# Kernel tuning notes

Measured on AMD Instinct MI355X. Metric: run time of the kernel, lower is better.

## Reference

```python
import jax, jax.numpy as jnp
import numpy as np

HEADS = 8
DIM_HEAD = 64
EPS = 1e-5

def setup_inputs() -> dict:
    key = jax.random.key(0)
    ks = jax.random.split(key, 5)
    c, inner = 320, HEADS * DIM_HEAD
    s = 0.02
    return {
        "hidden_states": jax.random.normal(ks[0], (4, c, 16, 32, 32), jnp.float32),
        "ln_w": jnp.ones((c,), jnp.float32),
        "ln_b": jnp.zeros((c,), jnp.float32),
        "Wq": jax.random.normal(ks[1], (inner, c), jnp.float32) * s,
        "Wk": jax.random.normal(ks[2], (inner, c), jnp.float32) * s,
        "Wv": jax.random.normal(ks[3], (inner, c), jnp.float32) * s,
        "Wo": jax.random.normal(ks[4], (c, inner), jnp.float32) * s,
        "bo": jnp.zeros((c,), jnp.float32),
    }

def reference(hidden_states, ln_w, ln_b, Wq, Wk, Wv, Wo, bo):
    b, c, t, h, w = hidden_states.shape
    scale = DIM_HEAD ** (-0.5)
    # (b h w) t c
    x0 = jnp.transpose(hidden_states, (0, 3, 4, 2, 1)).reshape(b * h * w, t, c)
    # LayerNorm over channel dim
    mu = jnp.mean(x0, axis=-1, keepdims=True)
    var = jnp.var(x0, axis=-1, keepdims=True)
    xn = (x0 - mu) / jnp.sqrt(var + EPS) * ln_w + ln_b
    # QKV projections (self-attention: encoder_hidden_states = normed hidden)
    q = xn @ Wq.T  # [B, t, inner]
    k = xn @ Wk.T
    v = xn @ Wv.T
    B = b * h * w
    q = q.reshape(B, t, HEADS, DIM_HEAD)
    k = k.reshape(B, t, HEADS, DIM_HEAD)
    v = v.reshape(B, t, HEADS, DIM_HEAD)
    scores = jnp.einsum("bqhd,bkhd->bhqk", q, k) * scale
    probs = jax.nn.softmax(scores, axis=-1)
    out = jnp.einsum("bhqk,bkhd->bqhd", probs, v).reshape(B, t, HEADS * DIM_HEAD)
    out = out @ Wo.T + bo
    out = out + x0  # residual (dropout p=0)
    # back to b c t h w
    return jnp.transpose(out.reshape(b, h, w, t, c), (0, 4, 3, 1, 2))
```

## Files before the change

kernel.cpp:

```cpp
#include <hip/hip_runtime.h>

#define TT 16
#define CC 320
#define NHEADS 8
#define DH 64
#define INNER 512

typedef float f32x4 __attribute__((ext_vector_type(4)));
typedef short bf16x8 __attribute__((ext_vector_type(8)));
typedef unsigned short u16;

__device__ __forceinline__ float bf2f(u16 u){
    union { unsigned int i; float f; } v; v.i = ((unsigned int)u) << 16; return v.f;
}
__device__ __forceinline__ u16 f2bf(float f){
    union { float f; unsigned int i; } v; v.f = f;
    unsigned int x = v.i;
    return (u16)((x + 0x7fffu + ((x >> 16) & 1u)) >> 16);
}

__global__ __launch_bounds__(256) void k_w2bf(const float* __restrict__ wq, const float* __restrict__ wk,
                                              const float* __restrict__ wv, const float* __restrict__ wo,
                                              u16* __restrict__ oq, u16* __restrict__ ok,
                                              u16* __restrict__ ov, u16* __restrict__ oo){
    const float* s; u16* d;
    switch (blockIdx.y){
        case 0: s = wq; d = oq; break;
        case 1: s = wk; d = ok; break;
        case 2: s = wv; d = ov; break;
        default: s = wo; d = oo; break;
    }
    int i = (blockIdx.x * 256 + threadIdx.x) * 4;
    f32x4 v = *(const f32x4*)(s + i);
    d[i + 0] = f2bf(v[0]); d[i + 1] = f2bf(v[1]);
    d[i + 2] = f2bf(v[2]); d[i + 3] = f2bf(v[3]);
}

__global__ __launch_bounds__(256) void k_ln(const float* __restrict__ x, const float* __restrict__ lnw,
                                            const float* __restrict__ lnb, u16* __restrict__ xn){
    __shared__ float tile[CC][37];
    __shared__ float psum[32][36];
    __shared__ float psq[32][36];
    __shared__ float meanb[32];
    __shared__ float rstdb[32];

    int wg = blockIdx.x;
    int t = wg & 15, h = (wg >> 4) & 31, b = wg >> 9;
    int tid = threadIdx.x;
    const size_t base = ((size_t)(b * CC) * TT + t) * 1024 + h * 32;

    int w4 = (tid & 7) * 4, cg = tid >> 3;
    f32x4 s4 = {0.f,0.f,0.f,0.f}, q4 = {0.f,0.f,0.f,0.f};
    for (int i = 0; i < 10; ++i){
        int c = cg * 10 + i;
        f32x4 v = *(const f32x4*)(x + base + (size_t)c * 16384 + w4);
        tile[c][w4 + 0] = v[0]; tile[c][w4 + 1] = v[1];
        tile[c][w4 + 2] = v[2]; tile[c][w4 + 3] = v[3];
        s4 += v; q4 += v * v;
    }
    psum[cg][w4 + 0] = s4[0]; psum[cg][w4 + 1] = s4[1]; psum[cg][w4 + 2] = s4[2]; psum[cg][w4 + 3] = s4[3];
    psq [cg][w4 + 0] = q4[0]; psq [cg][w4 + 1] = q4[1]; psq [cg][w4 + 2] = q4[2]; psq [cg][w4 + 3] = q4[3];
    __syncthreads();

    if (tid < 32){
        float s = 0.f, q = 0.f;
        for (int g = 0; g < 32; ++g){ s += psum[g][tid]; q += psq[g][tid]; }
        float mean = s * (1.f / CC);
        float var  = q * (1.f / CC) - mean * mean;
        meanb[tid] = mean;
        rstdb[tid] = rsqrtf(var + 1e-5f);
    }
    __syncthreads();

    int cl = tid & 63, wq_ = tid >> 6;
    float lw[5], lb[5];
    #pragma unroll
    for (int ci = 0; ci < 5; ++ci){ lw[ci] = lnw[ci * 64 + cl]; lb[ci] = lnb[ci * 64 + cl]; }
    int s_base = (b * 32 + h) * 32;
    for (int wi = 0; wi < 8; ++wi){
        int w = wq_ * 8 + wi;
        float mean = meanb[w], rstd = rstdb[w];
        size_t rowoff = ((size_t)(s_base + w) * TT + t) * CC;
        #pragma unroll
        for (int ci = 0; ci < 5; ++ci){
            int c = ci * 64 + cl;
            float nv = (tile[c][w] - mean) * rstd * lw[ci] + lb[ci];
            xn[rowoff + c] = f2bf(nv);
        }
    }
}

__global__ __launch_bounds__(256, 2) void k_attn(const u16* __restrict__ xng,
                                                 const u16* __restrict__ wq, const u16* __restrict__ wk,
                                                 const u16* __restrict__ wv, const u16* __restrict__ wo,
                                                 const float* __restrict__ bo, u16* __restrict__ proj){
    __shared__ u16 xn_s[64][328];
    __shared__ u16 qh_s[64][72];
    __shared__ u16 kh_s[64][72];
    __shared__ u16 vt_s[64][88];
    __shared__ u16 p_s[4][16][40];

    int tid = threadIdx.x;
    int lane = tid & 63;
    int wid = tid >> 6;
    int l15 = lane & 15;
    int g4  = lane >> 4;
    int s0 = blockIdx.x * 4;

    {
        const u16* src = xng + (size_t)s0 * TT * CC;
        #pragma unroll
        for (int i = 0; i < 10; ++i){
            int ch = tid + 256 * i;
            int r = ch / 40, cc8 = (ch % 40) * 8;
            *(bf16x8*)(&xn_s[r][cc8]) = *(const bf16x8*)(src + r * CC + cc8);
        }
        #pragma unroll
        for (int i = 0; i < 4; ++i){
            int idx = tid + 256 * i;
            vt_s[idx >> 4][64 + (idx & 15)] = 0;
        }
        #pragma unroll
        for (int i = 0; i < 4; ++i){
            int idx = tid + 256 * i;
            int wgg = idx >> 8, rest = idx & 255;
            p_s[wgg][rest >> 4][16 + (rest & 15)] = 0;
        }
    }
    __syncthreads();

    f32x4 acco[5][4];
    #pragma unroll
    for (int j = 0; j < 5; ++j)
        #pragma unroll
        for (int mb = 0; mb < 4; ++mb) acco[j][mb] = (f32x4){0.f,0.f,0.f,0.f};

    const f32x4 zero4 = (f32x4){0.f,0.f,0.f,0.f};

    for (int hd = 0; hd < NHEADS; ++hd){
        f32x4 aq[4], ak[4], av[4];
        #pragma unroll
        for (int mb = 0; mb < 4; ++mb){ aq[mb] = zero4; ak[mb] = zero4; av[mb] = zero4; }
        const u16* wqrow = wq + ((size_t)(hd * DH + wid * 16 + l15)) * CC + g4 * 8;
        const u16* wkrow = wk + ((size_t)(hd * DH + wid * 16 + l15)) * CC + g4 * 8;
        const u16* wvrow = wv + ((size_t)(hd * DH + wid * 16 + l15)) * CC + g4 * 8;
        for (int k0 = 0; k0 < CC; k0 += 32){
            bf16x8 bq = *(const bf16x8*)(wqrow + k0);
            bf16x8 bk = *(const bf16x8*)(wkrow + k0);
            bf16x8 aw = *(const bf16x8*)(wvrow + k0);
            #pragma unroll
            for (int mb = 0; mb < 4; ++mb){
                bf16x8 xa = *(const bf16x8*)(&xn_s[mb * 16 + l15][k0 + g4 * 8]);
                aq[mb] = __builtin_amdgcn_mfma_f32_16x16x32_bf16(xa, bq, aq[mb], 0, 0, 0);
                ak[mb] = __builtin_amdgcn_mfma_f32_16x16x32_bf16(xa, bk, ak[mb], 0, 0, 0);
                av[mb] = __builtin_amdgcn_mfma_f32_16x16x32_bf16(aw, xa, av[mb], 0, 0, 0);
            }
        }
        #pragma unroll
        for (int mb = 0; mb < 4; ++mb){
            #pragma unroll
            for (int r = 0; r < 4; ++r){
                int row = mb * 16 + g4 * 4 + r;
                qh_s[row][wid * 16 + l15] = f2bf(aq[mb][r] * 0.125f);
                kh_s[row][wid * 16 + l15] = f2bf(ak[mb][r]);
                vt_s[wid * 16 + g4 * 4 + r][mb * 16 + l15] = f2bf(av[mb][r]);
            }
        }
        __syncthreads();

        f32x4 sc = zero4;
        #pragma unroll
        for (int k0 = 0; k0 < DH; k0 += 32){
            bf16x8 qa = *(const bf16x8*)(&qh_s[wid * 16 + l15][k0 + g4 * 8]);
            bf16x8 kb = *(const bf16x8*)(&kh_s[wid * 16 + l15][k0 + g4 * 8]);
            sc = __builtin_amdgcn_mfma_f32_16x16x32_bf16(qa, kb, sc, 0, 0, 0);
        }
        f32x4 pr;
        #pragma unroll
        for (int r = 0; r < 4; ++r){
            float m = sc[r];
            m = fmaxf(m, __shfl_xor(m, 1)); m = fmaxf(m, __shfl_xor(m, 2));
            m = fmaxf(m, __shfl_xor(m, 4)); m = fmaxf(m, __shfl_xor(m, 8));
            float e = __expf(sc[r] - m);
            float s = e;
            s += __shfl_xor(s, 1); s += __shfl_xor(s, 2);
            s += __shfl_xor(s, 4); s += __shfl_xor(s, 8);
            pr[r] = e / s;
        }
        #pragma unroll
        for (int r = 0; r < 4; ++r) p_s[wid][g4 * 4 + r][l15] = f2bf(pr[r]);

        bf16x8 pa = *(const bf16x8*)(&p_s[wid][l15][g4 * 8]);
        f32x4 at[4];
        #pragma unroll
        for (int nb = 0; nb < 4; ++nb){
            bf16x8 vb = *(const bf16x8*)(&vt_s[nb * 16 + l15][wid * 16 + g4 * 8]);
            at[nb] = __builtin_amdgcn_mfma_f32_16x16x32_bf16(pa, vb, zero4, 0, 0, 0);
        }
        __syncthreads();
        #pragma unroll
        for (int nb = 0; nb < 4; ++nb)
            #pragma unroll
            for (int r = 0; r < 4; ++r)
                qh_s[wid * 16 + g4 * 4 + r][nb * 16 + l15] = f2bf(at[nb][r]);
        __syncthreads();

        #pragma unroll
        for (int k0 = 0; k0 < DH; k0 += 32){
            bf16x8 af[4];
            #pragma unroll
            for (int mb = 0; mb < 4; ++mb)
                af[mb] = *(const bf16x8*)(&qh_s[mb * 16 + l15][k0 + g4 * 8]);
            #pragma unroll
            for (int j = 0; j < 5; ++j){
                bf16x8 bw = *(const bf16x8*)(wo + ((size_t)((wid * 5 + j) * 16 + l15)) * INNER + hd * DH + k0 + g4 * 8);
                #pragma unroll
                for (int mb = 0; mb < 4; ++mb)
                    acco[j][mb] = __builtin_amdgcn_mfma_f32_16x16x32_bf16(af[mb], bw, acco[j][mb], 0, 0, 0);
            }
        }
        __syncthreads();
    }

    #pragma unroll
    for (int j = 0; j < 5; ++j){
        int c = (wid * 5 + j) * 16 + l15;
        float bias = bo[c];
        #pragma unroll
        for (int mb = 0; mb < 4; ++mb){
            size_t rowbase = ((size_t)(s0 + mb) * TT) * CC;
            #pragma unroll
            for (int r = 0; r < 4; ++r){
                int t = g4 * 4 + r;
                proj[rowbase + (size_t)t * CC + c] = f2bf(acco[j][mb][r] + bias);
            }
        }
    }
}

__global__ __launch_bounds__(256) void k_res(const u16* __restrict__ proj, const float* __restrict__ x,
                                             float* __restrict__ out){
    __shared__ u16 tile[32][328];
    int wg = blockIdx.x;
    int t = wg & 15, h = (wg >> 4) & 31, b = wg >> 9;
    int tid = threadIdx.x;
    int s0 = (b * 32 + h) * 32;
    #pragma unroll
    for (int i = 0; i < 5; ++i){
        int ch = tid + 256 * i;
        int w = ch / 40, cc8 = (ch % 40) * 8;
        *(bf16x8*)(&tile[w][cc8]) = *(const bf16x8*)(proj + ((size_t)(s0 + w) * TT + t) * CC + cc8);
    }
    __syncthreads();
    int w = tid & 31, cq = tid >> 5;
    size_t base = ((size_t)(b * CC) * TT + t) * 1024 + h * 32 + w;
    for (int i = 0; i < 40; ++i){
        int c = cq * 40 + i;
        size_t idx = base + (size_t)c * 16384;
        out[idx] = x[idx] + bf2f(tile[w][c]);
    }
}

extern "C" void kernel_launch(void* const* d_in, const int* in_sizes, int n_in,
                              void* d_out, int out_size, void* d_ws, size_t ws_size,
                              hipStream_t stream){
    const float* hid = (const float*)d_in[0];
    const float* lnw = (const float*)d_in[1];
    const float* lnb = (const float*)d_in[2];
    const float* Wq  = (const float*)d_in[3];
    const float* Wk  = (const float*)d_in[4];
    const float* Wv  = (const float*)d_in[5];
    const float* Wo  = (const float*)d_in[6];
    const float* bo  = (const float*)d_in[7];

    char* ws = (char*)d_ws;
    const size_t WN = 163840;
    u16* wq_b = (u16*)ws;
    u16* wk_b = wq_b + WN;
    u16* wv_b = wk_b + WN;
    u16* wo_b = wv_b + WN;
    u16* xn   = wo_b + WN;
    u16* proj = xn + (size_t)4096 * TT * CC;

    k_w2bf<<<dim3(160, 4), 256, 0, stream>>>(Wq, Wk, Wv, Wo, wq_b, wk_b, wv_b, wo_b);
    k_ln  <<<2048, 256, 0, stream>>>(hid, lnw, lnb, xn);
    k_attn<<<1024, 256, 0, stream>>>(xn, wq_b, wk_b, wv_b, wo_b, bo, proj);
    k_res <<<2048, 256, 0, stream>>>(proj, hid, (float*)d_out);
}
```

Measured before the change: 232.3 us.

## Retile attention kernel to 512 threads with register-resident xn fragments

The fused attention kernel now handles 8 sequences (128 rows) per 512-thread block. Each wave keeps its 32 rows of normalized input as register fragments, so there is no shared-memory staging of xn. Each wave computes a 32x32 tile of Q/K/V per head, which raises weight reuse per load. The per-head barrier count drops from four to three by writing the attention output into the K buffer, and the output projection is split into two column halves per wave. This costs many more registers per thread (20 A fragments plus 20 output accumulators) under a 2-blocks-per-CU bound of 512 threads, which risks spills or lower occupancy.

```diff
diff --git a/kernel.cpp b/kernel.cpp
--- a/kernel.cpp
+++ b/kernel.cpp
@@ -90,150 +90,177 @@
     }
 }
 
-__global__ __launch_bounds__(256, 2) void k_attn(const u16* __restrict__ xng,
+__global__ __launch_bounds__(512, 2) void k_attn(const u16* __restrict__ xng,
                                                  const u16* __restrict__ wq, const u16* __restrict__ wk,
                                                  const u16* __restrict__ wv, const u16* __restrict__ wo,
                                                  const float* __restrict__ bo, u16* __restrict__ proj){
-    __shared__ u16 xn_s[64][328];
-    __shared__ u16 qh_s[64][72];
-    __shared__ u16 kh_s[64][72];
-    __shared__ u16 vt_s[64][88];
-    __shared__ u16 p_s[4][16][40];
+    __shared__ u16 qh_s[128][76];
+    __shared__ u16 kh_s[128][76];
+    __shared__ u16 vt_s[64][148];
+    __shared__ u16 p_s[8][16][40];
 
     int tid = threadIdx.x;
     int lane = tid & 63;
     int wid = tid >> 6;
     int l15 = lane & 15;
     int g4  = lane >> 4;
-    int s0 = blockIdx.x * 4;
-
+    int mh = wid >> 1;
+    int nq = wid & 1;
+    const size_t mbase = (size_t)blockIdx.x * 128;
+
+    for (int i = tid; i < 64 * 20; i += 512) vt_s[i / 20][128 + i % 20] = 0;
+    for (int i = tid; i < 8 * 16 * 16; i += 512){
+        int w = i >> 8, rest = i & 255;
+        p_s[w][rest >> 4][16 + (rest & 15)] = 0;
+    }
+
+    bf16x8 a_f[2][10];
     {
-        const u16* src = xng + (size_t)s0 * TT * CC;
-        #pragma unroll
-        for (int i = 0; i < 10; ++i){
-            int ch = tid + 256 * i;
-            int r = ch / 40, cc8 = (ch % 40) * 8;
-            *(bf16x8*)(&xn_s[r][cc8]) = *(const bf16x8*)(src + r * CC + cc8);
-        }
-        #pragma unroll
-        for (int i = 0; i < 4; ++i){
-            int idx = tid + 256 * i;
-            vt_s[idx >> 4][64 + (idx & 15)] = 0;
-        }
-        #pragma unroll
-        for (int i = 0; i < 4; ++i){
-            int idx = tid + 256 * i;
-            int wgg = idx >> 8, rest = idx & 255;
-            p_s[wgg][rest >> 4][16 + (rest & 15)] = 0;
-        }
-    }
-    __syncthreads();
-
-    f32x4 acco[5][4];
+        const u16* xrow = xng + (mbase + mh * 32 + l15) * CC + g4 * 8;
+        #pragma unroll
+        for (int mb = 0; mb < 2; ++mb)
+            #pragma unroll
+            for (int kk = 0; kk < 10; ++kk)
+                a_f[mb][kk] = *(const bf16x8*)(xrow + mb * 16 * CC + kk * 32);
+    }
+
+    f32x4 acco[10][2];
     #pragma unroll
-    for (int j = 0; j < 5; ++j)
-        #pragma unroll
-        for (int mb = 0; mb < 4; ++mb) acco[j][mb] = (f32x4){0.f,0.f,0.f,0.f};
+    for (int j = 0; j < 10; ++j)
+        #pragma unroll
+        for (int mb = 0; mb < 2; ++mb) acco[j][mb] = (f32x4){0.f,0.f,0.f,0.f};
 
     const f32x4 zero4 = (f32x4){0.f,0.f,0.f,0.f};
 
     for (int hd = 0; hd < NHEADS; ++hd){
-        f32x4 aq[4], ak[4], av[4];
-        #pragma unroll
-        for (int mb = 0; mb < 4; ++mb){ aq[mb] = zero4; ak[mb] = zero4; av[mb] = zero4; }
-        const u16* wqrow = wq + ((size_t)(hd * DH + wid * 16 + l15)) * CC + g4 * 8;
-        const u16* wkrow = wk + ((size_t)(hd * DH + wid * 16 + l15)) * CC + g4 * 8;
-        const u16* wvrow = wv + ((size_t)(hd * DH + wid * 16 + l15)) * CC + g4 * 8;
-        for (int k0 = 0; k0 < CC; k0 += 32){
-            bf16x8 bq = *(const bf16x8*)(wqrow + k0);
-            bf16x8 bk = *(const bf16x8*)(wkrow + k0);
-            bf16x8 aw = *(const bf16x8*)(wvrow + k0);
-            #pragma unroll
-            for (int mb = 0; mb < 4; ++mb){
-                bf16x8 xa = *(const bf16x8*)(&xn_s[mb * 16 + l15][k0 + g4 * 8]);
-                aq[mb] = __builtin_amdgcn_mfma_f32_16x16x32_bf16(xa, bq, aq[mb], 0, 0, 0);
-                ak[mb] = __builtin_amdgcn_mfma_f32_16x16x32_bf16(xa, bk, ak[mb], 0, 0, 0);
-                av[mb] = __builtin_amdgcn_mfma_f32_16x16x32_bf16(aw, xa, av[mb], 0, 0, 0);
-            }
-        }
-        #pragma unroll
-        for (int mb = 0; mb < 4; ++mb){
+        f32x4 aq[2][2], ak[2][2];
+        #pragma unroll
+        for (int mb = 0; mb < 2; ++mb)
+            #pragma unroll
+            for (int nn = 0; nn < 2; ++nn){ aq[mb][nn] = zero4; ak[mb][nn] = zero4; }
+        {
+            const u16* wqb = wq + (size_t)(hd * DH + nq * 32 + l15) * CC + g4 * 8;
+            const u16* wkb = wk + (size_t)(hd * DH + nq * 32 + l15) * CC + g4 * 8;
+            #pragma unroll
+            for (int kk = 0; kk < 10; ++kk){
+                bf16x8 bq0 = *(const bf16x8*)(wqb + kk * 32);
+                bf16x8 bq1 = *(const bf16x8*)(wqb + 16 * CC + kk * 32);
+                bf16x8 bk0 = *(const bf16x8*)(wkb + kk * 32);
+                bf16x8 bk1 = *(const bf16x8*)(wkb + 16 * CC + kk * 32);
+                #pragma unroll
+                for (int mb = 0; mb < 2; ++mb){
+                    aq[mb][0] = __builtin_amdgcn_mfma_f32_16x16x32_bf16(a_f[mb][kk], bq0, aq[mb][0], 0, 0, 0);
+                    aq[mb][1] = __builtin_amdgcn_mfma_f32_16x16x32_bf16(a_f[mb][kk], bq1, aq[mb][1], 0, 0, 0);
+                    ak[mb][0] = __builtin_amdgcn_mfma_f32_16x16x32_bf16(a_f[mb][kk], bk0, ak[mb][0], 0, 0, 0);
+                    ak[mb][1] = __builtin_amdgcn_mfma_f32_16x16x32_bf16(a_f[mb][kk], bk1, ak[mb][1], 0, 0, 0);
+                }
+            }
+        }
+        f32x4 av[2][2];
+        #pragma unroll
+        for (int nn = 0; nn < 2; ++nn)
+            #pragma unroll
+            for (int mb = 0; mb < 2; ++mb) av[nn][mb] = zero4;
+        {
+            const u16* wvb = wv + (size_t)(hd * DH + nq * 32 + l15) * CC + g4 * 8;
+            #pragma unroll
+            for (int kk = 0; kk < 10; ++kk){
+                bf16x8 bv0 = *(const bf16x8*)(wvb + kk * 32);
+                bf16x8 bv1 = *(const bf16x8*)(wvb + 16 * CC + kk * 32);
+                #pragma unroll
+                for (int mb = 0; mb < 2; ++mb){
+                    av[0][mb] = __builtin_amdgcn_mfma_f32_16x16x32_bf16(bv0, a_f[mb][kk], av[0][mb], 0, 0, 0);
+                    av[1][mb] = __builtin_amdgcn_mfma_f32_16x16x32_bf16(bv1, a_f[mb][kk], av[1][mb], 0, 0, 0);
+                }
+            }
+        }
+
+        __syncthreads();
+        #pragma unroll
+        for (int mb = 0; mb < 2; ++mb)
+            #pragma unroll
+            for (int nn = 0; nn < 2; ++nn)
+                #pragma unroll
+                for (int r = 0; r < 4; ++r){
+                    int row = mh * 32 + mb * 16 + g4 * 4 + r;
+                    int col = nq * 32 + nn * 16 + l15;
+                    qh_s[row][col] = f2bf(aq[mb][nn][r] * 0.125f);
+                    kh_s[row][col] = f2bf(ak[mb][nn][r]);
+                }
+        #pragma unroll
+        for (int nn = 0; nn < 2; ++nn)
+            #pragma unroll
+            for (int mb = 0; mb < 2; ++mb)
+                #pragma unroll
+                for (int r = 0; r < 4; ++r)
+                    vt_s[nq * 32 + nn * 16 + g4 * 4 + r][mh * 32 + mb * 16 + l15] = f2bf(av[nn][mb][r]);
+        __syncthreads();
+
+        {
+            int s = wid;
+            f32x4 sc = zero4;
+            #pragma unroll
+            for (int k0 = 0; k0 < DH; k0 += 32){
+                bf16x8 qa = *(const bf16x8*)(&qh_s[s * 16 + l15][k0 + g4 * 8]);
+                bf16x8 kb = *(const bf16x8*)(&kh_s[s * 16 + l15][k0 + g4 * 8]);
+                sc = __builtin_amdgcn_mfma_f32_16x16x32_bf16(qa, kb, sc, 0, 0, 0);
+            }
+            f32x4 pr;
             #pragma unroll
             for (int r = 0; r < 4; ++r){
-                int row = mb * 16 + g4 * 4 + r;
-                qh_s[row][wid * 16 + l15] = f2bf(aq[mb][r] * 0.125f);
-                kh_s[row][wid * 16 + l15] = f2bf(ak[mb][r]);
-                vt_s[wid * 16 + g4 * 4 + r][mb * 16 + l15] = f2bf(av[mb][r]);
-            }
+                float m = sc[r];
+                m = fmaxf(m, __shfl_xor(m, 1)); m = fmaxf(m, __shfl_xor(m, 2));
+                m = fmaxf(m, __shfl_xor(m, 4)); m = fmaxf(m, __shfl_xor(m, 8));
+                float e = __expf(sc[r] - m);
+                float ss = e;
+                ss += __shfl_xor(ss, 1); ss += __shfl_xor(ss, 2);
+                ss += __shfl_xor(ss, 4); ss += __shfl_xor(ss, 8);
+                pr[r] = e / ss;
+            }
+            #pragma unroll
+            for (int r = 0; r < 4; ++r) p_s[s][g4 * 4 + r][l15] = f2bf(pr[r]);
+
+            bf16x8 pa = *(const bf16x8*)(&p_s[s][l15][g4 * 8]);
+            f32x4 at[4];
+            #pragma unroll
+            for (int nb = 0; nb < 4; ++nb){
+                bf16x8 vb = *(const bf16x8*)(&vt_s[nb * 16 + l15][s * 16 + g4 * 8]);
+                at[nb] = __builtin_amdgcn_mfma_f32_16x16x32_bf16(pa, vb, zero4, 0, 0, 0);
+            }
+            #pragma unroll
+            for (int nb = 0; nb < 4; ++nb)
+                #pragma unroll
+                for (int r = 0; r < 4; ++r)
+                    kh_s[s * 16 + g4 * 4 + r][nb * 16 + l15] = f2bf(at[nb][r]);
         }
         __syncthreads();
 
-        f32x4 sc = zero4;
         #pragma unroll
         for (int k0 = 0; k0 < DH; k0 += 32){
-            bf16x8 qa = *(const bf16x8*)(&qh_s[wid * 16 + l15][k0 + g4 * 8]);
-            bf16x8 kb = *(const bf16x8*)(&kh_s[wid * 16 + l15][k0 + g4 * 8]);
-            sc = __builtin_amdgcn_mfma_f32_16x16x32_bf16(qa, kb, sc, 0, 0, 0);
-        }
-        f32x4 pr;
-        #pragma unroll
-        for (int r = 0; r < 4; ++r){
-            float m = sc[r];
-            m = fmaxf(m, __shfl_xor(m, 1)); m = fmaxf(m, __shfl_xor(m, 2));
-            m = fmaxf(m, __shfl_xor(m, 4)); m = fmaxf(m, __shfl_xor(m, 8));
-            float e = __expf(sc[r] - m);
-            float s = e;
-            s += __shfl_xor(s, 1); s += __shfl_xor(s, 2);
-            s += __shfl_xor(s, 4); s += __shfl_xor(s, 8);
-            pr[r] = e / s;
-        }
-        #pragma unroll
-        for (int r = 0; r < 4; ++r) p_s[wid][g4 * 4 + r][l15] = f2bf(pr[r]);
-
-        bf16x8 pa = *(const bf16x8*)(&p_s[wid][l15][g4 * 8]);
-        f32x4 at[4];
-        #pragma unroll
-        for (int nb = 0; nb < 4; ++nb){
-            bf16x8 vb = *(const bf16x8*)(&vt_s[nb * 16 + l15][wid * 16 + g4 * 8]);
-            at[nb] = __builtin_amdgcn_mfma_f32_16x16x32_bf16(pa, vb, zero4, 0, 0, 0);
-        }
-        __syncthreads();
-        #pragma unroll
-        for (int nb = 0; nb < 4; ++nb)
+            bf16x8 af[2];
+            #pragma unroll
+            for (int mb = 0; mb < 2; ++mb)
+                af[mb] = *(const bf16x8*)(&kh_s[mh * 32 + mb * 16 + l15][k0 + g4 * 8]);
+            #pragma unroll
+            for (int j = 0; j < 10; ++j){
+                bf16x8 bw = *(const bf16x8*)(wo + (size_t)(nq * 160 + j * 16 + l15) * INNER + hd * DH + k0 + g4 * 8);
+                #pragma unroll
+                for (int mb = 0; mb < 2; ++mb)
+                    acco[j][mb] = __builtin_amdgcn_mfma_f32_16x16x32_bf16(af[mb], bw, acco[j][mb], 0, 0, 0);
+            }
+        }
+    }
+
+    #pragma unroll
+    for (int j = 0; j < 10; ++j){
+        int c = nq * 160 + j * 16 + l15;
+        float bias = bo[c];
+        #pragma unroll
+        for (int mb = 0; mb < 2; ++mb){
+            size_t row0 = mbase + mh * 32 + mb * 16 + g4 * 4;
             #pragma unroll
             for (int r = 0; r < 4; ++r)
-                qh_s[wid * 16 + g4 * 4 + r][nb * 16 + l15] = f2bf(at[nb][r]);
-        __syncthreads();
-
-        #pragma unroll
-        for (int k0 = 0; k0 < DH; k0 += 32){
-            bf16x8 af[4];
-            #pragma unroll
-            for (int mb = 0; mb < 4; ++mb)
-                af[mb] = *(const bf16x8*)(&qh_s[mb * 16 + l15][k0 + g4 * 8]);
-            #pragma unroll
-            for (int j = 0; j < 5; ++j){
-                bf16x8 bw = *(const bf16x8*)(wo + ((size_t)((wid * 5 + j) * 16 + l15)) * INNER + hd * DH + k0 + g4 * 8);
-                #pragma unroll
-                for (int mb = 0; mb < 4; ++mb)
-                    acco[j][mb] = __builtin_amdgcn_mfma_f32_16x16x32_bf16(af[mb], bw, acco[j][mb], 0, 0, 0);
-            }
-        }
-        __syncthreads();
-    }
-
-    #pragma unroll
-    for (int j = 0; j < 5; ++j){
-        int c = (wid * 5 + j) * 16 + l15;
-        float bias = bo[c];
-        #pragma unroll
-        for (int mb = 0; mb < 4; ++mb){
-            size_t rowbase = ((size_t)(s0 + mb) * TT) * CC;
-            #pragma unroll
-            for (int r = 0; r < 4; ++r){
-                int t = g4 * 4 + r;
-                proj[rowbase + (size_t)t * CC + c] = f2bf(acco[j][mb][r] + bias);
-            }
+                proj[(row0 + r) * CC + c] = f2bf(acco[j][mb][r] + bias);
         }
     }
 }
@@ -284,6 +311,6 @@
 
     k_w2bf<<<dim3(160, 4), 256, 0, stream>>>(Wq, Wk, Wv, Wo, wq_b, wk_b, wv_b, wo_b);
     k_ln  <<<2048, 256, 0, stream>>>(hid, lnw, lnb, xn);
-    k_attn<<<1024, 256, 0, stream>>>(xn, wq_b, wk_b, wv_b, wo_b, bo, proj);
+    k_attn<<<512, 512, 0, stream>>>(xn, wq_b, wk_b, wv_b, wo_b, bo, proj);
     k_res <<<2048, 256, 0, stream>>>(proj, hid, (float*)d_out);
 }
```

Measured after the change: 413.6 us. 78.1% more time.
